# Kernel tuning notes

Hardware: AMD Instinct MI355X
Metric: run time of the kernel (lower is better)

## Reference

```python
import jax, jax.numpy as jnp
import numpy as np

B, S, L = 256, 512, 128


def setup_inputs() -> dict:
    key = jax.random.key(0)
    k0, k1, k2, k3, k4, k5 = jax.random.split(key, 6)
    features = jax.random.normal(k0, (B, S, L), dtype=jnp.float32)
    attention_mask = jnp.ones((B, S), dtype=jnp.int32)  # all positions valid
    labels = jax.random.randint(k1, (B, S), 0, L)
    confidence = jax.random.uniform(k2, (B,), dtype=jnp.float32)
    start_transitions = jax.random.uniform(k3, (L,), minval=-0.1, maxval=0.1)
    end_transitions = jax.random.uniform(k4, (L,), minval=-0.1, maxval=0.1)
    transitions = jax.random.uniform(k5, (L, L), minval=-0.1, maxval=0.1)
    return {
        "features": features,
        "start_transitions": start_transitions,
        "end_transitions": end_transitions,
        "transitions": transitions,
        "confidence": confidence,
        "attention_mask": attention_mask,
        "labels": labels,
    }


def _crf_loss(features, start_transitions, end_transitions, transitions,
              confidence, attention_mask, labels):
    # time-major, matching torch.swapaxes(features, 0, 1)
    feats = jnp.swapaxes(features, 0, 1)                    # [S,B,L]
    mask = jnp.swapaxes(attention_mask, 0, 1).astype(bool)  # [S,B]
    labs = jnp.swapaxes(jnp.where(labels == -100, 0, labels), 0, 1)  # [S,B]
    bs = feats.shape[1]
    barange = jnp.arange(bs)

    # ---- log numerator (gold path score), fully vectorized over time ----
    emit = jnp.take_along_axis(feats, labs[:, :, None], axis=2)[..., 0]  # [S,B]
    trans_scores = transitions[labs[:-1], labs[1:]]                      # [S-1,B]
    maskf = mask[1:].astype(feats.dtype)
    log_num = (start_transitions[labs[0]] + emit[0]
               + jnp.sum((trans_scores + emit[1:]) * maskf, axis=0))
    seq_lens = mask.sum(axis=0) - 1                                      # [B]
    last_tags = labs[seq_lens, barange]
    log_num = log_num + end_transitions[last_tags]

    # ---- log denominator (partition function) via sequential scan ----
    def step(alpha, xs):
        feat_t, mask_t = xs  # [B,L], [B]
        nxt = jax.nn.logsumexp(
            alpha[:, :, None] + transitions[None, :, :] + feat_t[:, None, :],
            axis=1)
        return jnp.where(mask_t[:, None], nxt, alpha), None

    alpha0 = start_transitions + feats[0]                    # [B,L]
    alpha, _ = jax.lax.scan(step, alpha0, (feats[1:], mask[1:]))
    log_den = jax.nn.logsumexp(alpha + end_transitions, axis=1)  # [B]

    loss = (log_den - log_num) * confidence
    return jnp.mean(loss)


def reference(features, start_transitions, end_transitions, transitions,
              confidence, attention_mask, labels):
    return _crf_loss(features, start_transitions, end_transitions, transitions,
                     confidence, attention_mask, labels)
```

## Files before the change

kernel.cpp:

```cpp
#include <hip/hip_runtime.h>
#include <hip/hip_bf16.h>
#include <math.h>

#define NB 256
#define SS 512
#define LL 128

typedef short bf16x8 __attribute__((ext_vector_type(8)));
typedef float f32x4 __attribute__((ext_vector_type(4)));

__device__ __forceinline__ short f2bf(float f) {
    __hip_bfloat16 h = __float2bfloat16(f);
    short s;
    __builtin_memcpy(&s, &h, 2);
    return s;
}
__device__ __forceinline__ float bf2f(short s) {
    return __int_as_float(((int)(unsigned short)s) << 16);
}

#define MFMA1632(c, a, bb) \
    c = __builtin_amdgcn_mfma_f32_16x16x32_bf16(a, bb, c, 0, 0, 0)

__device__ __forceinline__ void wave_barrier() {
    asm volatile("s_waitcnt lgkmcnt(0)" ::: "memory");
    __builtin_amdgcn_s_barrier();
}

template <int ISB>
__device__ __forceinline__ void run_chain4(
    const int w, const int lane,
    const float* __restrict__ fb,
    const float* __restrict__ start_t,
    const float* __restrict__ end_t,
    const float* __restrict__ trans,
    short* __restrict__ img,
    float* __restrict__ eRing,
    const int* __restrict__ lmask,
    float* __restrict__ outv,
    float* __restrict__ oute)
{
    const int lo = lane & 15;
    const int hi = lane >> 4;
    const int nt0 = 2 * w, nt1 = 2 * w + 1;

    bf16x8 Af0[4], Af1[4];
#pragma unroll
    for (int kt = 0; kt < 4; ++kt) {
        bf16x8 f0, f1;
        const int n0 = 16 * nt0 + lo, n1 = 16 * nt1 + lo;
#pragma unroll
        for (int j = 0; j < 8; ++j) {
            const int k = 32 * kt + 8 * hi + j;
            f0[j] = f2bf(__expf(ISB ? trans[n0 * LL + k] : trans[k * LL + n0]));
            f1[j] = f2bf(__expf(ISB ? trans[n1 * LL + k] : trans[k * LL + n1]));
        }
        Af0[kt] = f0;
        Af1[kt] = f1;
    }

    float v[2][4];
#pragma unroll
    for (int n2 = 0; n2 < 2; ++n2)
#pragma unroll
        for (int j = 0; j < 4; ++j) {
            const int p = 16 * (2 * w + n2) + 4 * hi + j;
            v[n2][j] = ISB ? __expf(end_t[p]) : __expf(start_t[p] + fb[p]);
        }

    f32x4 ep0 = {1.f, 1.f, 1.f, 1.f}, ep1 = ep0;
    if (ISB) {
#pragma unroll
        for (int j = 0; j < 4; ++j) {
            ep0[j] = __expf(fb[(size_t)511 * LL + 16 * nt0 + 4 * hi + j]);
            ep1[j] = __expf(fb[(size_t)511 * LL + 16 * nt1 + 4 * hi + j]);
        }
    }

    float2 nxt;
    {
        const int row = ISB ? (508 - w) : (w + 3);
        nxt = *(const float2*)(fb + (size_t)row * LL + 2 * lane);
    }

    wave_barrier();

    int eacc = 0;

    for (int r = 0; r < 256; ++r) {
        short4 p0, p1;
        p0.x = f2bf(ISB ? v[0][0] * ep0[0] : v[0][0]);
        p0.y = f2bf(ISB ? v[0][1] * ep0[1] : v[0][1]);
        p0.z = f2bf(ISB ? v[0][2] * ep0[2] : v[0][2]);
        p0.w = f2bf(ISB ? v[0][3] * ep0[3] : v[0][3]);
        p1.x = f2bf(ISB ? v[1][0] * ep1[0] : v[1][0]);
        p1.y = f2bf(ISB ? v[1][1] * ep1[1] : v[1][1]);
        p1.z = f2bf(ISB ? v[1][2] * ep1[2] : v[1][2]);
        p1.w = f2bf(ISB ? v[1][3] * ep1[3] : v[1][3]);
        short* ib = img + (r & 1) * LL;
        if (lo == 0) {
            *(short4*)(ib + 32 * w + 4 * hi) = p0;
            *(short4*)(ib + 32 * w + 16 + 4 * hi) = p1;
        }
        wave_barrier();

        bf16x8 Bf[4];
#pragma unroll
        for (int kt = 0; kt < 4; ++kt)
            Bf[kt] = *(const bf16x8*)(ib + 32 * kt + 8 * hi);

        const float* rp = eRing + (r & 3) * LL + 4 * hi;
        f32x4 ec0 = *(const f32x4*)(rp + 16 * nt0);
        f32x4 ec1 = *(const f32x4*)(rp + 16 * nt1);

        if (w == (r & 3)) {
            *(float2*)(eRing + ((r + 2) & 3) * LL + 2 * lane) =
                make_float2(__expf(nxt.x), __expf(nxt.y));
            const int rowN = ISB ? (504 - r) : (r + 7);
            nxt = *(const float2*)(fb + (size_t)rowN * LL + 2 * lane);
        }

        int mt = lmask[ISB ? (511 - r) : (r + 1)];
        if (!ISB && r == 255) mt = 0;

        f32x4 cc0 = {0.f, 0.f, 0.f, 0.f}, cc1 = {0.f, 0.f, 0.f, 0.f};
#pragma unroll
        for (int kt = 0; kt < 4; ++kt) {
            MFMA1632(cc0, Af0[kt], Bf[kt]);
            MFMA1632(cc1, Af1[kt], Bf[kt]);
        }

#pragma unroll
        for (int j = 0; j < 4; ++j) {
            const float c0 = ISB ? cc0[j] : ec0[j] * cc0[j];
            const float c1 = ISB ? cc1[j] : ec1[j] * cc1[j];
            v[0][j] = mt ? c0 : v[0][j];
            v[1][j] = mt ? c1 : v[1][j];
        }

        if ((r & 7) == 7) {
            float s = 0.f;
#pragma unroll
            for (int kt = 0; kt < 4; ++kt)
#pragma unroll
                for (int j = 0; j < 8; ++j) s += bf2f(Bf[kt][j]);
            s += __shfl_xor(s, 16);
            s += __shfl_xor(s, 32);
            int ex;
            frexpf(s, &ex);
#pragma unroll
            for (int n2 = 0; n2 < 2; ++n2)
#pragma unroll
                for (int j = 0; j < 4; ++j) v[n2][j] = ldexpf(v[n2][j], -ex);
            eacc += ex;
        }

        if (ISB) { ep0 = ec0; ep1 = ec1; }
    }

    if (lo == 0) {
        *(f32x4*)(outv + 16 * nt0 + 4 * hi) =
            (f32x4){v[0][0], v[0][1], v[0][2], v[0][3]};
        *(f32x4*)(outv + 16 * nt1 + 4 * hi) =
            (f32x4){v[1][0], v[1][1], v[1][2], v[1][3]};
    }
    if (w == 0 && lane == 0) *oute = (float)eacc;
}

__global__ __launch_bounds__(256, 2) void crf_chain_kernel(
    const float* __restrict__ feats,
    const float* __restrict__ start_t,
    const float* __restrict__ end_t,
    const float* __restrict__ trans,
    const int* __restrict__ mask,
    const int* __restrict__ labels,
    float* __restrict__ ws)
{
    const int bid = blockIdx.x;
    const int b = bid & 255;
    const int isB = bid >> 8;
    const int tid = threadIdx.x;
    const int w = tid >> 6;
    const int lane = tid & 63;

    __shared__ __align__(16) short img[2 * LL];
    __shared__ __align__(16) float eRing[4 * LL];
    __shared__ int lmask[SS];
    __shared__ float nred[4];
    __shared__ int cred[4];

    const float* fb = feats + (size_t)b * SS * LL;

    lmask[tid] = mask[b * SS + tid];
    lmask[tid + 256] = mask[b * SS + tid + 256];
    {
        const int slot = tid >> 7;
        const int e = tid & 127;
        const int row = isB ? (510 - slot) : (1 + slot);
        eRing[slot * LL + e] = __expf(fb[(size_t)row * LL + e]);
    }

    float* av = ws;
    float* bv = ws + NB * LL;
    float* eFa = ws + 2 * NB * LL;
    float* eBa = eFa + NB;
    float* lognum = eBa + NB;

    if (isB)
        run_chain4<1>(w, lane, fb, start_t, end_t, trans, img, eRing, lmask,
                      bv + b * LL, eBa + b);
    else
        run_chain4<0>(w, lane, fb, start_t, end_t, trans, img, eRing, lmask,
                      av + b * LL, eFa + b);

    if (isB) {
        const int* lb = labels + b * SS;
        const int* mb = mask + b * SS;
        float term = 0.f;
        int cnt = 0;
#pragma unroll
        for (int q = 0; q < 2; ++q) {
            const int tt = tid + 256 * q;
            int l = lb[tt];
            if ((unsigned)l >= LL) l = 0;
            const int m = mb[tt];
            cnt += (m != 0);
            if (tt == 0) {
                term += start_t[l] + fb[l];
            } else if (m) {
                int lp = lb[tt - 1];
                if ((unsigned)lp >= LL) lp = 0;
                term += trans[lp * LL + l] + fb[(size_t)tt * LL + l];
            }
        }
#pragma unroll
        for (int o = 1; o < 64; o <<= 1) {
            term += __shfl_xor(term, o);
            cnt += __shfl_xor(cnt, o);
        }
        if (lane == 0) { nred[w] = term; cred[w] = cnt; }
        __syncthreads();
        if (tid == 0) {
            const float tot = nred[0] + nred[1] + nred[2] + nred[3];
            const int c = cred[0] + cred[1] + cred[2] + cred[3];
            int sl = c - 1;
            sl = sl < 0 ? 0 : (sl >= SS ? SS - 1 : sl);
            int lt = lb[sl];
            if ((unsigned)lt >= LL) lt = 0;
            lognum[b] = tot + end_t[lt];
        }
    }
}

__global__ __launch_bounds__(256) void crf_final_kernel(
    const float* __restrict__ ws, const float* __restrict__ conf,
    float* __restrict__ out)
{
    const int tid = threadIdx.x;
    const float* av = ws;
    const float* bv = ws + NB * LL;
    const float* eFa = ws + 2 * NB * LL;
    const float* eBa = eFa + NB;
    const float* ln = eBa + NB;

    const float4* a4 = (const float4*)(av + tid * LL);
    const float4* b4 = (const float4*)(bv + tid * LL);
    float dot = 0.f;
#pragma unroll 8
    for (int k = 0; k < 32; ++k) {
        float4 a = a4[k], bb = b4[k];
        dot += a.x * bb.x + a.y * bb.y + a.z * bb.z + a.w * bb.w;
    }
    float logZ = logf(dot) + 0.69314718055994531f * (eFa[tid] + eBa[tid]);
    float loss = (logZ - ln[tid]) * conf[tid] * (1.0f / NB);

#pragma unroll
    for (int o = 1; o < 64; o <<= 1) loss += __shfl_xor(loss, o);
    __shared__ float red[4];
    if ((tid & 63) == 0) red[tid >> 6] = loss;
    __syncthreads();
    if (tid == 0) out[0] = red[0] + red[1] + red[2] + red[3];
}

extern "C" void kernel_launch(void* const* d_in, const int* in_sizes, int n_in,
                              void* d_out, int out_size, void* d_ws, size_t ws_size,
                              hipStream_t stream) {
    const float* feats  = (const float*)d_in[0];
    const float* startt = (const float*)d_in[1];
    const float* endt   = (const float*)d_in[2];
    const float* trans  = (const float*)d_in[3];
    const float* conf   = (const float*)d_in[4];
    const int*   mask   = (const int*)d_in[5];
    const int*   labels = (const int*)d_in[6];
    float* out = (float*)d_out;
    float* ws = (float*)d_ws;

    hipLaunchKernelGGL(crf_chain_kernel, dim3(2 * NB), dim3(256), 0, stream,
                       feats, startt, endt, trans, mask, labels, ws);
    hipLaunchKernelGGL(crf_final_kernel, dim3(1), dim3(256), 0, stream,
                       ws, conf, out);
}
```

Baseline: 205.6 us.

## Pack two sequences per block as MFMA columns, eight waves one tile each

Each block now runs the forward or backward recursion for two batch elements at once. The two state vectors become the two column groups of the MFMA B operand, and each of eight waves owns one 16-row tile instead of two. The shared-memory exp ring is replaced by per-lane register prefetch of the next feature rows with exp computed inline. This halves the grid and doubles the threads per block, aiming to cut serial MFMA work per wave and use the idle B columns. In exchange it adds redundant exp work and uses larger, fewer blocks.

Result: slower. 243.3 us (+18.3%).

```diff
diff --git a/kernel.cpp b/kernel.cpp
--- a/kernel.cpp
+++ b/kernel.cpp
@@ -28,80 +28,65 @@
 }
 
 template <int ISB>
-__device__ __forceinline__ void run_chain4(
+__device__ __forceinline__ void run_chain_pair(
     const int w, const int lane,
-    const float* __restrict__ fb,
+    const float* __restrict__ fb0,
+    const float* __restrict__ fb1,
     const float* __restrict__ start_t,
     const float* __restrict__ end_t,
     const float* __restrict__ trans,
     short* __restrict__ img,
-    float* __restrict__ eRing,
-    const int* __restrict__ lmask,
+    const int* __restrict__ lmask2,
     float* __restrict__ outv,
-    float* __restrict__ oute)
+    float* __restrict__ oute,
+    const int b0, const int b1)
 {
     const int lo = lane & 15;
     const int hi = lane >> 4;
-    const int nt0 = 2 * w, nt1 = 2 * w + 1;
-
-    bf16x8 Af0[4], Af1[4];
+    const int colg = lo >> 3;
+    const float* fbl = colg ? fb1 : fb0;
+
+    bf16x8 Af[4];
 #pragma unroll
     for (int kt = 0; kt < 4; ++kt) {
-        bf16x8 f0, f1;
-        const int n0 = 16 * nt0 + lo, n1 = 16 * nt1 + lo;
+        bf16x8 fr;
+        const int n = 16 * w + lo;
 #pragma unroll
         for (int j = 0; j < 8; ++j) {
             const int k = 32 * kt + 8 * hi + j;
-            f0[j] = f2bf(__expf(ISB ? trans[n0 * LL + k] : trans[k * LL + n0]));
-            f1[j] = f2bf(__expf(ISB ? trans[n1 * LL + k] : trans[k * LL + n1]));
-        }
-        Af0[kt] = f0;
-        Af1[kt] = f1;
-    }
-
-    float v[2][4];
-#pragma unroll
-    for (int n2 = 0; n2 < 2; ++n2)
-#pragma unroll
-        for (int j = 0; j < 4; ++j) {
-            const int p = 16 * (2 * w + n2) + 4 * hi + j;
-            v[n2][j] = ISB ? __expf(end_t[p]) : __expf(start_t[p] + fb[p]);
-        }
-
-    f32x4 ep0 = {1.f, 1.f, 1.f, 1.f}, ep1 = ep0;
+            fr[j] = f2bf(__expf(ISB ? trans[n * LL + k] : trans[k * LL + n]));
+        }
+        Af[kt] = fr;
+    }
+
+    float v[4];
+#pragma unroll
+    for (int j = 0; j < 4; ++j) {
+        const int p = 16 * w + 4 * hi + j;
+        v[j] = ISB ? __expf(end_t[p]) : __expf(start_t[p] + fbl[p]);
+    }
+
+    f32x4 ep = {1.f, 1.f, 1.f, 1.f};
     if (ISB) {
 #pragma unroll
-        for (int j = 0; j < 4; ++j) {
-            ep0[j] = __expf(fb[(size_t)511 * LL + 16 * nt0 + 4 * hi + j]);
-            ep1[j] = __expf(fb[(size_t)511 * LL + 16 * nt1 + 4 * hi + j]);
-        }
-    }
-
-    float2 nxt;
-    {
-        const int row = ISB ? (508 - w) : (w + 3);
-        nxt = *(const float2*)(fb + (size_t)row * LL + 2 * lane);
-    }
-
-    wave_barrier();
+        for (int j = 0; j < 4; ++j)
+            ep[j] = __expf(fbl[(size_t)511 * LL + 16 * w + 4 * hi + j]);
+    }
+
+    f32x4 cur = *(const f32x4*)(fbl + (size_t)(ISB ? 510 : 1) * LL + 16 * w + 4 * hi);
+    f32x4 nxt = *(const f32x4*)(fbl + (size_t)(ISB ? 509 : 2) * LL + 16 * w + 4 * hi);
 
     int eacc = 0;
 
     for (int r = 0; r < 256; ++r) {
-        short4 p0, p1;
-        p0.x = f2bf(ISB ? v[0][0] * ep0[0] : v[0][0]);
-        p0.y = f2bf(ISB ? v[0][1] * ep0[1] : v[0][1]);
-        p0.z = f2bf(ISB ? v[0][2] * ep0[2] : v[0][2]);
-        p0.w = f2bf(ISB ? v[0][3] * ep0[3] : v[0][3]);
-        p1.x = f2bf(ISB ? v[1][0] * ep1[0] : v[1][0]);
-        p1.y = f2bf(ISB ? v[1][1] * ep1[1] : v[1][1]);
-        p1.z = f2bf(ISB ? v[1][2] * ep1[2] : v[1][2]);
-        p1.w = f2bf(ISB ? v[1][3] * ep1[3] : v[1][3]);
-        short* ib = img + (r & 1) * LL;
-        if (lo == 0) {
-            *(short4*)(ib + 32 * w + 4 * hi) = p0;
-            *(short4*)(ib + 32 * w + 16 + 4 * hi) = p1;
-        }
+        short4 pk;
+        pk.x = f2bf(ISB ? v[0] * ep[0] : v[0]);
+        pk.y = f2bf(ISB ? v[1] * ep[1] : v[1]);
+        pk.z = f2bf(ISB ? v[2] * ep[2] : v[2]);
+        pk.w = f2bf(ISB ? v[3] * ep[3] : v[3]);
+        short* ib = img + (r & 1) * 2 * LL + colg * LL;
+        if ((lo & 7) == 0)
+            *(short4*)(ib + 16 * w + 4 * hi) = pk;
         wave_barrier();
 
         bf16x8 Bf[4];
@@ -109,33 +94,26 @@
         for (int kt = 0; kt < 4; ++kt)
             Bf[kt] = *(const bf16x8*)(ib + 32 * kt + 8 * hi);
 
-        const float* rp = eRing + (r & 3) * LL + 4 * hi;
-        f32x4 ec0 = *(const f32x4*)(rp + 16 * nt0);
-        f32x4 ec1 = *(const f32x4*)(rp + 16 * nt1);
-
-        if (w == (r & 3)) {
-            *(float2*)(eRing + ((r + 2) & 3) * LL + 2 * lane) =
-                make_float2(__expf(nxt.x), __expf(nxt.y));
-            const int rowN = ISB ? (504 - r) : (r + 7);
-            nxt = *(const float2*)(fb + (size_t)rowN * LL + 2 * lane);
-        }
-
-        int mt = lmask[ISB ? (511 - r) : (r + 1)];
+        f32x4 eftv;
+#pragma unroll
+        for (int j = 0; j < 4; ++j) eftv[j] = __expf(cur[j]);
+        cur = nxt;
+        {
+            const int rowN = ISB ? (508 - r) : (r + 3);
+            nxt = *(const f32x4*)(fbl + (size_t)rowN * LL + 16 * w + 4 * hi);
+        }
+
+        int mt = lmask2[colg * SS + (ISB ? (511 - r) : (r + 1))];
         if (!ISB && r == 255) mt = 0;
 
-        f32x4 cc0 = {0.f, 0.f, 0.f, 0.f}, cc1 = {0.f, 0.f, 0.f, 0.f};
-#pragma unroll
-        for (int kt = 0; kt < 4; ++kt) {
-            MFMA1632(cc0, Af0[kt], Bf[kt]);
-            MFMA1632(cc1, Af1[kt], Bf[kt]);
-        }
+        f32x4 cc = {0.f, 0.f, 0.f, 0.f};
+#pragma unroll
+        for (int kt = 0; kt < 4; ++kt) MFMA1632(cc, Af[kt], Bf[kt]);
 
 #pragma unroll
         for (int j = 0; j < 4; ++j) {
-            const float c0 = ISB ? cc0[j] : ec0[j] * cc0[j];
-            const float c1 = ISB ? cc1[j] : ec1[j] * cc1[j];
-            v[0][j] = mt ? c0 : v[0][j];
-            v[1][j] = mt ? c1 : v[1][j];
+            const float cand = ISB ? cc[j] : eftv[j] * cc[j];
+            v[j] = mt ? cand : v[j];
         }
 
         if ((r & 7) == 7) {
@@ -149,25 +127,22 @@
             int ex;
             frexpf(s, &ex);
 #pragma unroll
-            for (int n2 = 0; n2 < 2; ++n2)
-#pragma unroll
-                for (int j = 0; j < 4; ++j) v[n2][j] = ldexpf(v[n2][j], -ex);
+            for (int j = 0; j < 4; ++j) v[j] = ldexpf(v[j], -ex);
             eacc += ex;
         }
 
-        if (ISB) { ep0 = ec0; ep1 = ec1; }
-    }
-
-    if (lo == 0) {
-        *(f32x4*)(outv + 16 * nt0 + 4 * hi) =
-            (f32x4){v[0][0], v[0][1], v[0][2], v[0][3]};
-        *(f32x4*)(outv + 16 * nt1 + 4 * hi) =
-            (f32x4){v[1][0], v[1][1], v[1][2], v[1][3]};
-    }
-    if (w == 0 && lane == 0) *oute = (float)eacc;
-}
-
-__global__ __launch_bounds__(256, 2) void crf_chain_kernel(
+        if (ISB) ep = eftv;
+    }
+
+    if (lo == 0)
+        *(f32x4*)(outv + b0 * LL + 16 * w + 4 * hi) = (f32x4){v[0], v[1], v[2], v[3]};
+    if (lo == 8)
+        *(f32x4*)(outv + b1 * LL + 16 * w + 4 * hi) = (f32x4){v[0], v[1], v[2], v[3]};
+    if (w == 0 && lane == 0) oute[b0] = (float)eacc;
+    if (w == 0 && lane == 8) oute[b1] = (float)eacc;
+}
+
+__global__ __launch_bounds__(512, 2) void crf_chain_kernel(
     const float* __restrict__ feats,
     const float* __restrict__ start_t,
     const float* __restrict__ end_t,
@@ -177,28 +152,23 @@
     float* __restrict__ ws)
 {
     const int bid = blockIdx.x;
-    const int b = bid & 255;
-    const int isB = bid >> 8;
+    const int isB = bid >> 7;
+    const int p = bid & 127;
+    const int b0 = 2 * p, b1 = 2 * p + 1;
     const int tid = threadIdx.x;
     const int w = tid >> 6;
     const int lane = tid & 63;
 
-    __shared__ __align__(16) short img[2 * LL];
-    __shared__ __align__(16) float eRing[4 * LL];
-    __shared__ int lmask[SS];
-    __shared__ float nred[4];
-    __shared__ int cred[4];
-
-    const float* fb = feats + (size_t)b * SS * LL;
-
-    lmask[tid] = mask[b * SS + tid];
-    lmask[tid + 256] = mask[b * SS + tid + 256];
-    {
-        const int slot = tid >> 7;
-        const int e = tid & 127;
-        const int row = isB ? (510 - slot) : (1 + slot);
-        eRing[slot * LL + e] = __expf(fb[(size_t)row * LL + e]);
-    }
+    __shared__ __align__(16) short img[2 * 2 * LL];
+    __shared__ int lmask2[2 * SS];
+    __shared__ float nred[8];
+    __shared__ int cred[8];
+
+    const float* fb0 = feats + (size_t)b0 * SS * LL;
+    const float* fb1 = feats + (size_t)b1 * SS * LL;
+
+    lmask2[tid] = mask[b0 * SS + tid];
+    lmask2[SS + tid] = mask[b1 * SS + tid];
 
     float* av = ws;
     float* bv = ws + NB * LL;
@@ -207,30 +177,32 @@
     float* lognum = eBa + NB;
 
     if (isB)
-        run_chain4<1>(w, lane, fb, start_t, end_t, trans, img, eRing, lmask,
-                      bv + b * LL, eBa + b);
+        run_chain_pair<1>(w, lane, fb0, fb1, start_t, end_t, trans, img, lmask2,
+                          bv, eBa, b0, b1);
     else
-        run_chain4<0>(w, lane, fb, start_t, end_t, trans, img, eRing, lmask,
-                      av + b * LL, eFa + b);
+        run_chain_pair<0>(w, lane, fb0, fb1, start_t, end_t, trans, img, lmask2,
+                          av, eFa, b0, b1);
 
     if (isB) {
-        const int* lb = labels + b * SS;
-        const int* mb = mask + b * SS;
+        const int bb = (w < 4) ? b0 : b1;
+        const float* fbn = (w < 4) ? fb0 : fb1;
+        const int* lb = labels + bb * SS;
+        const int* mb = mask + bb * SS;
         float term = 0.f;
         int cnt = 0;
 #pragma unroll
         for (int q = 0; q < 2; ++q) {
-            const int tt = tid + 256 * q;
+            const int tt = (w & 3) * 128 + lane + 64 * q;
             int l = lb[tt];
             if ((unsigned)l >= LL) l = 0;
             const int m = mb[tt];
             cnt += (m != 0);
             if (tt == 0) {
-                term += start_t[l] + fb[l];
+                term += start_t[l] + fbn[l];
             } else if (m) {
                 int lp = lb[tt - 1];
                 if ((unsigned)lp >= LL) lp = 0;
-                term += trans[lp * LL + l] + fb[(size_t)tt * LL + l];
+                term += trans[lp * LL + l] + fbn[(size_t)tt * LL + l];
             }
         }
 #pragma unroll
@@ -245,9 +217,18 @@
             const int c = cred[0] + cred[1] + cred[2] + cred[3];
             int sl = c - 1;
             sl = sl < 0 ? 0 : (sl >= SS ? SS - 1 : sl);
-            int lt = lb[sl];
+            int lt = labels[b0 * SS + sl];
             if ((unsigned)lt >= LL) lt = 0;
-            lognum[b] = tot + end_t[lt];
+            lognum[b0] = tot + end_t[lt];
+        }
+        if (tid == 256) {
+            const float tot = nred[4] + nred[5] + nred[6] + nred[7];
+            const int c = cred[4] + cred[5] + cred[6] + cred[7];
+            int sl = c - 1;
+            sl = sl < 0 ? 0 : (sl >= SS ? SS - 1 : sl);
+            int lt = labels[b1 * SS + sl];
+            if ((unsigned)lt >= LL) lt = 0;
+            lognum[b1] = tot + end_t[lt];
         }
     }
 }
@@ -295,7 +276,7 @@
     float* out = (float*)d_out;
     float* ws = (float*)d_ws;
 
-    hipLaunchKernelGGL(crf_chain_kernel, dim3(2 * NB), dim3(256), 0, stream,
+    hipLaunchKernelGGL(crf_chain_kernel, dim3(NB), dim3(512), 0, stream,
                        feats, startt, endt, trans, mask, labels, ws);
     hipLaunchKernelGGL(crf_final_kernel, dim3(1), dim3(256), 0, stream,
                        ws, conf, out);
```

## Split each CRF chain across eight waves with one MFMA tile per wave

Applied to the files above, without the earlier changes.

Each CRF forward/backward chain block now has 512 threads (8 waves) instead of 4. Each wave owns one 16-column output tile and issues 4 MFMAs per step instead of 8. This is meant to halve the serial MFMA latency on each step's critical path. The cost is a barrier across twice as many waves every step and lower per-CU block occupancy at 512 threads.

New measurement: 203.4 us. Within noise of the previous version (-1.1%).

```diff
diff --git a/kernel.cpp b/kernel.cpp
--- a/kernel.cpp
+++ b/kernel.cpp
@@ -28,7 +28,7 @@
 }
 
 template <int ISB>
-__device__ __forceinline__ void run_chain4(
+__device__ __forceinline__ void run_chain8(
     const int w, const int lane,
     const float* __restrict__ fb,
     const float* __restrict__ start_t,
@@ -42,43 +42,36 @@
 {
     const int lo = lane & 15;
     const int hi = lane >> 4;
-    const int nt0 = 2 * w, nt1 = 2 * w + 1;
-
-    bf16x8 Af0[4], Af1[4];
+
+    bf16x8 Af[4];
 #pragma unroll
     for (int kt = 0; kt < 4; ++kt) {
-        bf16x8 f0, f1;
-        const int n0 = 16 * nt0 + lo, n1 = 16 * nt1 + lo;
+        bf16x8 fr;
+        const int n = 16 * w + lo;
 #pragma unroll
         for (int j = 0; j < 8; ++j) {
             const int k = 32 * kt + 8 * hi + j;
-            f0[j] = f2bf(__expf(ISB ? trans[n0 * LL + k] : trans[k * LL + n0]));
-            f1[j] = f2bf(__expf(ISB ? trans[n1 * LL + k] : trans[k * LL + n1]));
-        }
-        Af0[kt] = f0;
-        Af1[kt] = f1;
-    }
-
-    float v[2][4];
-#pragma unroll
-    for (int n2 = 0; n2 < 2; ++n2)
-#pragma unroll
-        for (int j = 0; j < 4; ++j) {
-            const int p = 16 * (2 * w + n2) + 4 * hi + j;
-            v[n2][j] = ISB ? __expf(end_t[p]) : __expf(start_t[p] + fb[p]);
-        }
-
-    f32x4 ep0 = {1.f, 1.f, 1.f, 1.f}, ep1 = ep0;
+            fr[j] = f2bf(__expf(ISB ? trans[n * LL + k] : trans[k * LL + n]));
+        }
+        Af[kt] = fr;
+    }
+
+    float v[4];
+#pragma unroll
+    for (int j = 0; j < 4; ++j) {
+        const int p = 16 * w + 4 * hi + j;
+        v[j] = ISB ? __expf(end_t[p]) : __expf(start_t[p] + fb[p]);
+    }
+
+    f32x4 ep = {1.f, 1.f, 1.f, 1.f};
     if (ISB) {
 #pragma unroll
-        for (int j = 0; j < 4; ++j) {
-            ep0[j] = __expf(fb[(size_t)511 * LL + 16 * nt0 + 4 * hi + j]);
-            ep1[j] = __expf(fb[(size_t)511 * LL + 16 * nt1 + 4 * hi + j]);
-        }
-    }
-
-    float2 nxt;
-    {
+        for (int j = 0; j < 4; ++j)
+            ep[j] = __expf(fb[(size_t)511 * LL + 16 * w + 4 * hi + j]);
+    }
+
+    float2 nxt = make_float2(0.f, 0.f);
+    if (w < 4) {
         const int row = ISB ? (508 - w) : (w + 3);
         nxt = *(const float2*)(fb + (size_t)row * LL + 2 * lane);
     }
@@ -88,20 +81,14 @@
     int eacc = 0;
 
     for (int r = 0; r < 256; ++r) {
-        short4 p0, p1;
-        p0.x = f2bf(ISB ? v[0][0] * ep0[0] : v[0][0]);
-        p0.y = f2bf(ISB ? v[0][1] * ep0[1] : v[0][1]);
-        p0.z = f2bf(ISB ? v[0][2] * ep0[2] : v[0][2]);
-        p0.w = f2bf(ISB ? v[0][3] * ep0[3] : v[0][3]);
-        p1.x = f2bf(ISB ? v[1][0] * ep1[0] : v[1][0]);
-        p1.y = f2bf(ISB ? v[1][1] * ep1[1] : v[1][1]);
-        p1.z = f2bf(ISB ? v[1][2] * ep1[2] : v[1][2]);
-        p1.w = f2bf(ISB ? v[1][3] * ep1[3] : v[1][3]);
+        short4 pk;
+        pk.x = f2bf(ISB ? v[0] * ep[0] : v[0]);
+        pk.y = f2bf(ISB ? v[1] * ep[1] : v[1]);
+        pk.z = f2bf(ISB ? v[2] * ep[2] : v[2]);
+        pk.w = f2bf(ISB ? v[3] * ep[3] : v[3]);
         short* ib = img + (r & 1) * LL;
-        if (lo == 0) {
-            *(short4*)(ib + 32 * w + 4 * hi) = p0;
-            *(short4*)(ib + 32 * w + 16 + 4 * hi) = p1;
-        }
+        if (lo == 0)
+            *(short4*)(ib + 16 * w + 4 * hi) = pk;
         wave_barrier();
 
         bf16x8 Bf[4];
@@ -110,8 +97,7 @@
             Bf[kt] = *(const bf16x8*)(ib + 32 * kt + 8 * hi);
 
         const float* rp = eRing + (r & 3) * LL + 4 * hi;
-        f32x4 ec0 = *(const f32x4*)(rp + 16 * nt0);
-        f32x4 ec1 = *(const f32x4*)(rp + 16 * nt1);
+        f32x4 ec = *(const f32x4*)(rp + 16 * w);
 
         if (w == (r & 3)) {
             *(float2*)(eRing + ((r + 2) & 3) * LL + 2 * lane) =
@@ -123,19 +109,15 @@
         int mt = lmask[ISB ? (511 - r) : (r + 1)];
         if (!ISB && r == 255) mt = 0;
 
-        f32x4 cc0 = {0.f, 0.f, 0.f, 0.f}, cc1 = {0.f, 0.f, 0.f, 0.f};
-#pragma unroll
-        for (int kt = 0; kt < 4; ++kt) {
-            MFMA1632(cc0, Af0[kt], Bf[kt]);
-            MFMA1632(cc1, Af1[kt], Bf[kt]);
-        }
+        f32x4 cc = {0.f, 0.f, 0.f, 0.f};
+#pragma unroll
+        for (int kt = 0; kt < 4; ++kt)
+            MFMA1632(cc, Af[kt], Bf[kt]);
 
 #pragma unroll
         for (int j = 0; j < 4; ++j) {
-            const float c0 = ISB ? cc0[j] : ec0[j] * cc0[j];
-            const float c1 = ISB ? cc1[j] : ec1[j] * cc1[j];
-            v[0][j] = mt ? c0 : v[0][j];
-            v[1][j] = mt ? c1 : v[1][j];
+            const float cand = ISB ? cc[j] : ec[j] * cc[j];
+            v[j] = mt ? cand : v[j];
         }
 
         if ((r & 7) == 7) {
@@ -149,25 +131,19 @@
             int ex;
             frexpf(s, &ex);
 #pragma unroll
-            for (int n2 = 0; n2 < 2; ++n2)
-#pragma unroll
-                for (int j = 0; j < 4; ++j) v[n2][j] = ldexpf(v[n2][j], -ex);
+            for (int j = 0; j < 4; ++j) v[j] = ldexpf(v[j], -ex);
             eacc += ex;
         }
 
-        if (ISB) { ep0 = ec0; ep1 = ec1; }
-    }
-
-    if (lo == 0) {
-        *(f32x4*)(outv + 16 * nt0 + 4 * hi) =
-            (f32x4){v[0][0], v[0][1], v[0][2], v[0][3]};
-        *(f32x4*)(outv + 16 * nt1 + 4 * hi) =
-            (f32x4){v[1][0], v[1][1], v[1][2], v[1][3]};
-    }
+        if (ISB) ep = ec;
+    }
+
+    if (lo == 0)
+        *(f32x4*)(outv + 16 * w + 4 * hi) = (f32x4){v[0], v[1], v[2], v[3]};
     if (w == 0 && lane == 0) *oute = (float)eacc;
 }
 
-__global__ __launch_bounds__(256, 2) void crf_chain_kernel(
+__global__ __launch_bounds__(512, 2) void crf_chain_kernel(
     const float* __restrict__ feats,
     const float* __restrict__ start_t,
     const float* __restrict__ end_t,
@@ -192,8 +168,7 @@
     const float* fb = feats + (size_t)b * SS * LL;
 
     lmask[tid] = mask[b * SS + tid];
-    lmask[tid + 256] = mask[b * SS + tid + 256];
-    {
+    if (tid < 256) {
         const int slot = tid >> 7;
         const int e = tid & 127;
         const int row = isB ? (510 - slot) : (1 + slot);
@@ -207,38 +182,40 @@
     float* lognum = eBa + NB;
 
     if (isB)
-        run_chain4<1>(w, lane, fb, start_t, end_t, trans, img, eRing, lmask,
+        run_chain8<1>(w, lane, fb, start_t, end_t, trans, img, eRing, lmask,
                       bv + b * LL, eBa + b);
     else
-        run_chain4<0>(w, lane, fb, start_t, end_t, trans, img, eRing, lmask,
+        run_chain8<0>(w, lane, fb, start_t, end_t, trans, img, eRing, lmask,
                       av + b * LL, eFa + b);
 
     if (isB) {
         const int* lb = labels + b * SS;
         const int* mb = mask + b * SS;
-        float term = 0.f;
-        int cnt = 0;
-#pragma unroll
-        for (int q = 0; q < 2; ++q) {
-            const int tt = tid + 256 * q;
-            int l = lb[tt];
-            if ((unsigned)l >= LL) l = 0;
-            const int m = mb[tt];
-            cnt += (m != 0);
-            if (tt == 0) {
-                term += start_t[l] + fb[l];
-            } else if (m) {
-                int lp = lb[tt - 1];
-                if ((unsigned)lp >= LL) lp = 0;
-                term += trans[lp * LL + l] + fb[(size_t)tt * LL + l];
+        if (w < 4) {
+            float term = 0.f;
+            int cnt = 0;
+#pragma unroll
+            for (int q = 0; q < 2; ++q) {
+                const int tt = tid + 256 * q;
+                int l = lb[tt];
+                if ((unsigned)l >= LL) l = 0;
+                const int m = mb[tt];
+                cnt += (m != 0);
+                if (tt == 0) {
+                    term += start_t[l] + fb[l];
+                } else if (m) {
+                    int lp = lb[tt - 1];
+                    if ((unsigned)lp >= LL) lp = 0;
+                    term += trans[lp * LL + l] + fb[(size_t)tt * LL + l];
+                }
             }
-        }
-#pragma unroll
-        for (int o = 1; o < 64; o <<= 1) {
-            term += __shfl_xor(term, o);
-            cnt += __shfl_xor(cnt, o);
-        }
-        if (lane == 0) { nred[w] = term; cred[w] = cnt; }
+#pragma unroll
+            for (int o = 1; o < 64; o <<= 1) {
+                term += __shfl_xor(term, o);
+                cnt += __shfl_xor(cnt, o);
+            }
+            if (lane == 0) { nred[w] = term; cred[w] = cnt; }
+        }
         __syncthreads();
         if (tid == 0) {
             const float tot = nred[0] + nred[1] + nred[2] + nred[3];
@@ -295,7 +272,7 @@
     float* out = (float*)d_out;
     float* ws = (float*)d_ws;
 
-    hipLaunchKernelGGL(crf_chain_kernel, dim3(2 * NB), dim3(256), 0, stream,
+    hipLaunchKernelGGL(crf_chain_kernel, dim3(2 * NB), dim3(512), 0, stream,
                        feats, startt, endt, trans, mask, labels, ws);
     hipLaunchKernelGGL(crf_final_kernel, dim3(1), dim3(256), 0, stream,
                        ws, conf, out);
```
